# Optimization experiments

Hardware: AMD Instinct MI355X
Metric: run time of the kernel (lower is better)

Reference implementation:

```python
import jax, jax.numpy as jnp
import numpy as np

HEADS = 16
DIM_HEAD = 64
SCALE = DIM_HEAD ** -0.5


def setup_inputs() -> dict:
    key = jax.random.key(0)
    ks = jax.random.split(key, 5)
    dim = 1024
    inner = HEADS * DIM_HEAD  # 1024
    x = jax.random.normal(ks[0], (2, 2048, dim), dtype=jnp.float32)
    # Linear weights stored as [in, out] so y = x @ W
    s = dim ** -0.5
    Wq = jax.random.normal(ks[1], (dim, inner), dtype=jnp.float32) * s
    Wk = jax.random.normal(ks[2], (dim, inner), dtype=jnp.float32) * s
    Wv = jax.random.normal(ks[3], (dim, inner), dtype=jnp.float32) * s
    Wo = jax.random.normal(ks[4], (inner, dim), dtype=jnp.float32) * s
    bo = jnp.zeros((dim,), dtype=jnp.float32)
    return {"x": x, "Wq": Wq, "Wk": Wk, "Wv": Wv, "Wo": Wo, "bo": bo}


def reference(x, Wq, Wk, Wv, Wo, bo):
    b, n, _ = x.shape
    def split_heads(t):  # [b, n, h*d] -> [b, h, n, d]
        return t.reshape(b, n, HEADS, DIM_HEAD).transpose(0, 2, 1, 3)
    q = split_heads(x @ Wq)
    k = split_heads(x @ Wk)
    v = split_heads(x @ Wv)
    sim = jnp.einsum('bhid,bhjd->bhij', q, k) * SCALE  # [b, h, n, n]
    attn = jax.nn.softmax(sim, axis=-1)
    out = jnp.einsum('bhij,bhjd->bhid', attn, v)  # [b, h, n, d]
    out = out.transpose(0, 2, 1, 3).reshape(b, n, HEADS * DIM_HEAD)
    return out @ Wo + bo
```

## Files before the change

### kernel.cpp

```cpp
#include <hip/hip_runtime.h>
#include <hip/hip_fp16.h>

typedef _Float16 f16;
typedef __attribute__((ext_vector_type(8))) _Float16 half8;
typedef __attribute__((ext_vector_type(2))) __fp16 fp16x2_native;
typedef __attribute__((ext_vector_type(4))) float floatx4;
typedef __attribute__((ext_vector_type(16))) float f32x16;
typedef __attribute__((ext_vector_type(4))) unsigned uint4v;
typedef __attribute__((ext_vector_type(2))) unsigned uint2v;

static constexpr int DIM = 1024;
static constexpr int SEQ = 2048;
static constexpr int DH = 64;
static constexpr int MTOT = 4096;

__device__ __forceinline__ float fexp2(float x) {
#if __has_builtin(__builtin_amdgcn_exp2f)
  return __builtin_amdgcn_exp2f(x);
#else
  return exp2f(x);
#endif
}

__device__ __forceinline__ unsigned pkrtz(float a, float b) {
  fp16x2_native h = __builtin_amdgcn_cvt_pkrtz(a, b);
  return __builtin_bit_cast(unsigned, h);
}

__device__ __forceinline__ void pl32swap(unsigned& a, unsigned& b) {
#if __has_builtin(__builtin_amdgcn_permlane32_swap)
  uint2v r = __builtin_amdgcn_permlane32_swap(a, b, false, false);
  a = r.x;
  b = r.y;
#else
  asm volatile("v_permlane32_swap_b32 %0, %1" : "+v"(a), "+v"(b));
#endif
}

__device__ __forceinline__ void gll16(const f16* g, f16* l) {
  auto gp = (__attribute__((address_space(1))) unsigned*)(uintptr_t)(const void*)g;
  auto lp = (__attribute__((address_space(3))) unsigned*)(uintptr_t)(void*)l;
  __builtin_amdgcn_global_load_lds(gp, lp, 16, 0, 0);
}

__global__ __launch_bounds__(256) void k_transpose(
    const float* __restrict__ Wq, const float* __restrict__ Wk,
    const float* __restrict__ Wv, const float* __restrict__ Wo,
    f16* __restrict__ wt)
{
  __shared__ float tile[32][33];
  const int z = blockIdx.z;
  const float* W = (z == 0) ? Wq : (z == 1) ? Wk : (z == 2) ? Wv : Wo;
  f16* out = wt + (size_t)z * DIM * DIM;
  const int tx = threadIdx.x, ty = threadIdx.y;
  const int x0 = blockIdx.x * 32, y0 = blockIdx.y * 32;
#pragma unroll
  for (int i = 0; i < 4; ++i)
    tile[ty + i * 8][tx] = W[(size_t)(y0 + ty + i * 8) * DIM + (x0 + tx)];
  __syncthreads();
#pragma unroll
  for (int i = 0; i < 4; ++i)
    out[(size_t)(x0 + ty + i * 8) * DIM + (y0 + tx)] = (f16)tile[tx][ty + i * 8];
}

__global__ __launch_bounds__(256) void k_xcast(
    const float* __restrict__ in, f16* __restrict__ out)
{
  const int i = blockIdx.x * 256 + threadIdx.x;
  const float4* p = (const float4*)in;
  float4 a = p[2 * i], b = p[2 * i + 1];
  half8 h = {(f16)a.x, (f16)a.y, (f16)a.z, (f16)a.w,
             (f16)b.x, (f16)b.y, (f16)b.z, (f16)b.w};
  *(half8*)(out + (size_t)i * 8) = h;
}

__global__ __launch_bounds__(256) void k_vtrans(
    const f16* __restrict__ vh, f16* __restrict__ vt)
{
  __shared__ f16 T[64][72];
  const int tid = threadIdx.x;
  const int nt = blockIdx.x, bh = blockIdx.y;
  const int b = bh >> 4, h = bh & 15;
  const int n0 = nt * 64;
  const f16* src = vh + (size_t)b * SEQ * DIM + (size_t)h * DH;
#pragma unroll
  for (int i = 0; i < 2; ++i) {
    const int n = (tid >> 3) + i * 32;
    const int cc = tid & 7;
    half8 v = *(const half8*)(src + (size_t)(n0 + n) * DIM + cc * 8);
#pragma unroll
    for (int j = 0; j < 8; ++j) T[cc * 8 + j][n] = v[j];
  }
  __syncthreads();
  f16* dst = vt + (size_t)bh * DH * SEQ;
#pragma unroll
  for (int i = 0; i < 2; ++i) {
    const int d = (tid >> 3) + i * 32;
    const int cc = tid & 7;
    half8 w = *(const half8*)&T[d][cc * 8];
    *(half8*)(dst + (size_t)d * SEQ + n0 + cc * 8) = w;
  }
}

template <bool OUT_F32>
__global__ __launch_bounds__(256) void k_gemm2(
    const f16* __restrict__ A, const f16* __restrict__ BT,
    void* __restrict__ Cptr, const float* __restrict__ bias,
    int M, int N, int K, size_t bt_zstride, size_t c_zstride)
{
  __shared__ f16 SB[2][8192];

  const int tid = threadIdx.x;
  const int lane = tid & 63;
  const int wid = tid >> 6;
  const int wr = (wid >> 1) * 64, wc = (wid & 1) * 64;
  const int li = lane & 15, lg = lane >> 4;

  const f16* BTz = BT + (size_t)blockIdx.z * bt_zstride;
  const int row0 = blockIdx.x * 128, col0 = blockIdx.y * 128;

  const int c0 = tid;
  const int c1 = 256 + tid;
  const f16* a0 = A + (size_t)(row0 + (c0 >> 2)) * K + (c0 & 3) * 8;
  const f16* a1 = A + (size_t)(row0 + (c1 >> 2)) * K + (c1 & 3) * 8;
  const f16* b0 = BTz + (size_t)(col0 + (c0 >> 2)) * K + (c0 & 3) * 8;
  const f16* b1 = BTz + (size_t)(col0 + (c1 >> 2)) * K + (c1 & 3) * 8;
  const int da0 = wid * 512, da1 = 2048 + wid * 512;

  const floatx4 zero4 = {0.f, 0.f, 0.f, 0.f};
  floatx4 acc[4][4];
#pragma unroll
  for (int m = 0; m < 4; ++m)
#pragma unroll
    for (int n = 0; n < 4; ++n) acc[m][n] = zero4;

  auto issue = [&](int buf) {
    gll16(a0, &SB[buf][da0]);
    gll16(a1, &SB[buf][da1]);
    gll16(b0, &SB[buf][4096 + da0]);
    gll16(b1, &SB[buf][4096 + da1]);
    a0 += 32; a1 += 32; b0 += 32; b1 += 32;
  };

  const int nstep = K >> 5;
  issue(0);

  auto step = [&](int buf, int t) {
    asm volatile("s_waitcnt vmcnt(0)" ::: "memory");
    __builtin_amdgcn_s_barrier();
    asm volatile("" ::: "memory");
    if (t + 1 < nstep) issue(buf ^ 1);
    const f16* As = &SB[buf][0];
    const f16* Bs = &SB[buf][4096];
    half8 af[4], bf[4];
#pragma unroll
    for (int m = 0; m < 4; ++m)
      af[m] = *(const half8*)&As[(wr + m * 16 + li) * 32 + lg * 8];
#pragma unroll
    for (int n = 0; n < 4; ++n)
      bf[n] = *(const half8*)&Bs[(wc + n * 16 + li) * 32 + lg * 8];
#pragma unroll
    for (int m = 0; m < 4; ++m)
#pragma unroll
      for (int n = 0; n < 4; ++n)
        acc[m][n] = __builtin_amdgcn_mfma_f32_16x16x32_f16(af[m], bf[n], acc[m][n], 0, 0, 0);
  };

  for (int t2 = 0; t2 < nstep; t2 += 2) {
    step(0, t2);
    step(1, t2 + 1);
  }

#pragma unroll
  for (int m = 0; m < 4; ++m)
#pragma unroll
    for (int n = 0; n < 4; ++n)
#pragma unroll
      for (int r = 0; r < 4; ++r) {
        const int row = row0 + wr + m * 16 + lg * 4 + r;
        const int col = col0 + wc + n * 16 + li;
        if constexpr (OUT_F32) {
          float* C = (float*)Cptr + (size_t)blockIdx.z * c_zstride;
          C[(size_t)row * N + col] = acc[m][n][r] + bias[col];
        } else {
          f16* C = (f16*)Cptr + (size_t)blockIdx.z * c_zstride;
          C[(size_t)row * N + col] = (f16)acc[m][n][r];
        }
      }
}

__global__ __launch_bounds__(256) void k_attn3(
    const f16* __restrict__ qh, const f16* __restrict__ kh,
    const f16* __restrict__ vt, f16* __restrict__ oh)
{
  __shared__ f16 KV[2][8192];
  __shared__ float bc[4][32];

  const int tid = threadIdx.x;
  const int lane = tid & 63;
  const int wid = tid >> 6;
  const int col = lane & 31;
  const int hi = lane >> 5;

  const int id = blockIdx.x;
  const int xcd = id & 7;
  const int j = id >> 3;
  const int bh = xcd * 4 + (j >> 4);
  const int qi = j & 15;
  const int b = bh >> 4, h = bh & 15;

  const int q0 = qi * 128 + wid * 32;
  const size_t xbase = (size_t)b * SEQ * DIM + (size_t)h * DH;
  const size_t vtbase = (size_t)bh * DH * SEQ;

  const float SC = 0.125f * 1.44269504089f;
  const float RTRAW = 8.0f / SC;

  const int c0 = tid;
  const int c1 = 256 + tid;
  const int r0 = c0 >> 3, s0 = ((c0 & 7) ^ (r0 & 7)) * 8;
  const int r1 = c1 >> 3, s1 = ((c1 & 7) ^ (r1 & 7)) * 8;
  const f16* ks0 = kh + xbase + (size_t)r0 * DIM + s0;
  const f16* ks1 = kh + xbase + (size_t)r1 * DIM + s1;
  const f16* vs0 = vt + vtbase + (size_t)r0 * SEQ + s0;
  const f16* vs1 = vt + vtbase + (size_t)r1 * SEQ + s1;
  const int dk0 = wid * 512, dk1 = 2048 + wid * 512;

  auto issue = [&](int buf) {
    gll16(ks0, &KV[buf][dk0]);
    gll16(ks1, &KV[buf][dk1]);
    gll16(vs0, &KV[buf][4096 + dk0]);
    gll16(vs1, &KV[buf][4096 + dk1]);
    ks0 += 64 * DIM; ks1 += 64 * DIM; vs0 += 64; vs1 += 64;
  };

  half8 qb[4];
  {
    const f16* qrow = qh + xbase + (size_t)(q0 + col) * DIM;
#pragma unroll
    for (int s = 0; s < 4; ++s) qb[s] = *(const half8*)(qrow + s * 16 + hi * 8);
  }

  f32x16 o0 = {0, 0, 0, 0, 0, 0, 0, 0, 0, 0, 0, 0, 0, 0, 0, 0};
  f32x16 o1 = {0, 0, 0, 0, 0, 0, 0, 0, 0, 0, 0, 0, 0, 0, 0, 0};
  float m = -1e30f, lsum = 0.f;

  issue(0);

  auto tile = [&](int buf, int t) {
    asm volatile("s_waitcnt vmcnt(0)" ::: "memory");
    __builtin_amdgcn_s_barrier();
    asm volatile("" ::: "memory");
    if (t < 31) issue(buf ^ 1);
    const f16* Ks = &KV[buf][0];
    const f16* Vs = &KV[buf][4096];

#pragma unroll
    for (int kvs = 0; kvs < 2; ++kvs) {
      const int krow = kvs * 32 + col;
      f32x16 sacc = {0, 0, 0, 0, 0, 0, 0, 0, 0, 0, 0, 0, 0, 0, 0, 0};
      __builtin_amdgcn_s_setprio(1);
#pragma unroll
      for (int s = 0; s < 4; ++s) {
        const int cc = (2 * s + hi) ^ (krow & 7);
        half8 ka = *(const half8*)&Ks[krow * 64 + cc * 8];
        sacc = __builtin_amdgcn_mfma_f32_32x32x16_f16(ka, qb[s], sacc, 0, 0, 0);
      }
      __builtin_amdgcn_s_setprio(0);

      float smax = sacc[0];
#pragma unroll
      for (int r = 1; r < 16; ++r) smax = fmaxf(smax, sacc[r]);
      smax = fmaxf(smax, __shfl_xor(smax, 32));

      if (!__all(smax <= m + RTRAW)) {
        const float mn = fmaxf(m, smax);
        const float alpha = fexp2((m - mn) * SC);
        m = mn;
        lsum *= alpha;
        if (hi == 0) bc[wid][col] = alpha;
#pragma unroll
        for (int r = 0; r < 16; ++r) {
          const float a2 = bc[wid][(r & 3) + 8 * (r >> 2) + 4 * hi];
          o0[r] *= a2;
          o1[r] *= a2;
        }
      }

      const float mc = m * SC;
      float pw[16];
      float rs = 0.f;
#pragma unroll
      for (int r = 0; r < 16; ++r) {
        pw[r] = fexp2(fmaf(sacc[r], SC, -mc));
        rs += pw[r];
      }
      rs += __shfl_xor(rs, 32);
      lsum += rs;

      __builtin_amdgcn_s_setprio(1);
#pragma unroll
      for (int s2 = 0; s2 < 2; ++s2) {
        const int rb = s2 * 8;
        unsigned X0 = pkrtz(pw[rb + 0], pw[rb + 1]);
        unsigned X1 = pkrtz(pw[rb + 2], pw[rb + 3]);
        unsigned Y0 = pkrtz(pw[rb + 4], pw[rb + 5]);
        unsigned Y1 = pkrtz(pw[rb + 6], pw[rb + 7]);
        pl32swap(X0, Y0);
        pl32swap(X1, Y1);
        const half8 paf = __builtin_bit_cast(half8, (uint4v){X0, X1, Y0, Y1});
        const int kc = kvs * 4 + s2 * 2 + hi;
#pragma unroll
        for (int dt = 0; dt < 2; ++dt) {
          const int vrow = dt * 32 + col;
          const int cc = kc ^ (vrow & 7);
          half8 vb = *(const half8*)&Vs[vrow * 64 + cc * 8];
          if (dt == 0)
            o0 = __builtin_amdgcn_mfma_f32_32x32x16_f16(paf, vb, o0, 0, 0, 0);
          else
            o1 = __builtin_amdgcn_mfma_f32_32x32x16_f16(paf, vb, o1, 0, 0, 0);
        }
      }
      __builtin_amdgcn_s_setprio(0);
    }
  };

  for (int t2 = 0; t2 < 32; t2 += 2) {
    tile(0, t2);
    tile(1, t2 + 1);
  }

  const float inv = 1.0f / lsum;
  if (hi == 0) bc[wid][col] = inv;
#pragma unroll
  for (int r = 0; r < 16; ++r) {
    const int qr = (r & 3) + 8 * (r >> 2) + 4 * hi;
    const float iv = bc[wid][qr];
    f16* orow = oh + xbase + (size_t)(q0 + qr) * DIM;
    orow[col] = (f16)(o0[r] * iv);
    orow[32 + col] = (f16)(o1[r] * iv);
  }
}

extern "C" void kernel_launch(void* const* d_in, const int* in_sizes, int n_in,
                              void* d_out, int out_size, void* d_ws, size_t ws_size,
                              hipStream_t stream)
{
  const float* x  = (const float*)d_in[0];
  const float* Wq = (const float*)d_in[1];
  const float* Wk = (const float*)d_in[2];
  const float* Wv = (const float*)d_in[3];
  const float* Wo = (const float*)d_in[4];
  const float* bo = (const float*)d_in[5];

  char* ws = (char*)d_ws;
  f16* wt   = (f16*)ws;
  f16* qkvh = (f16*)(ws + (size_t)8 * 1024 * 1024);
  f16* ohp  = (f16*)(ws + (size_t)32 * 1024 * 1024);
  f16* vtb  = (f16*)(ws + (size_t)40 * 1024 * 1024);
  f16* xh   = ohp;

  k_transpose<<<dim3(32, 32, 4), dim3(32, 8), 0, stream>>>(Wq, Wk, Wv, Wo, wt);

  k_xcast<<<2048, 256, 0, stream>>>(x, xh);

  k_gemm2<false><<<dim3(32, 8, 3), 256, 0, stream>>>(
      xh, wt, qkvh, nullptr, MTOT, DIM, DIM,
      (size_t)DIM * DIM, (size_t)MTOT * DIM);

  k_vtrans<<<dim3(32, 32), 256, 0, stream>>>(
      qkvh + (size_t)2 * MTOT * DIM, vtb);

  k_attn3<<<512, 256, 0, stream>>>(
      qkvh, qkvh + (size_t)MTOT * DIM, vtb, ohp);

  k_gemm2<true><<<dim3(32, 8, 1), 256, 0, stream>>>(
      ohp, wt + (size_t)3 * DIM * DIM, d_out, bo, MTOT, DIM, DIM, 0, 0);
}
```

Baseline: 124.0 us.

## Split attention KV range across two wave groups and merge partial softmax

The attention kernel doubles its block to 512 threads. Two groups of four waves each process half of the key/value sequence for the same 128 query rows, with double-buffered shared memory enlarged to hold both halves. Afterwards the partial outputs, maxima and sums are combined through shared memory (split-K style). This is meant to raise wave occupancy and latency hiding on the 512-block grid. The cost is more shared memory, a final merge pass with an extra fp16 rounding of one partial, and a reduction tree rewrite for max and sum.

```diff
diff --git a/kernel.cpp b/kernel.cpp
--- a/kernel.cpp
+++ b/kernel.cpp
@@ -189,16 +189,19 @@
       }
 }
 
-__global__ __launch_bounds__(256) void k_attn3(
+__global__ __launch_bounds__(512) void k_attn4(
     const f16* __restrict__ qh, const f16* __restrict__ kh,
     const f16* __restrict__ vt, f16* __restrict__ oh)
 {
-  __shared__ f16 KV[2][8192];
-  __shared__ float bc[4][32];
+  __shared__ f16 KV[2][16384];
+  __shared__ float bc[8][32];
+  __shared__ float Lm[4][32], Ll[4][32], W0[4][32], W1[4][32];
 
   const int tid = threadIdx.x;
   const int lane = tid & 63;
   const int wid = tid >> 6;
+  const int g = wid >> 2;
+  const int sub = wid & 3;
   const int col = lane & 31;
   const int hi = lane >> 5;
 
@@ -209,28 +212,27 @@
   const int qi = j & 15;
   const int b = bh >> 4, h = bh & 15;
 
-  const int q0 = qi * 128 + wid * 32;
+  const int q0 = qi * 128 + sub * 32;
   const size_t xbase = (size_t)b * SEQ * DIM + (size_t)h * DH;
   const size_t vtbase = (size_t)bh * DH * SEQ;
 
   const float SC = 0.125f * 1.44269504089f;
   const float RTRAW = 8.0f / SC;
 
-  const int c0 = tid;
-  const int c1 = 256 + tid;
-  const int r0 = c0 >> 3, s0 = ((c0 & 7) ^ (r0 & 7)) * 8;
-  const int r1 = c1 >> 3, s1 = ((c1 & 7) ^ (r1 & 7)) * 8;
-  const f16* ks0 = kh + xbase + (size_t)r0 * DIM + s0;
-  const f16* ks1 = kh + xbase + (size_t)r1 * DIM + s1;
-  const f16* vs0 = vt + vtbase + (size_t)r0 * SEQ + s0;
-  const f16* vs1 = vt + vtbase + (size_t)r1 * SEQ + s1;
-  const int dk0 = wid * 512, dk1 = 2048 + wid * 512;
+  const int lc = tid & 511;
+  const int srow = lc >> 3;
+  const int sw = ((lc & 7) ^ (srow & 7)) * 8;
+  const f16* ks0 = kh + xbase + (size_t)srow * DIM + sw;
+  const f16* ks1 = kh + xbase + (size_t)(1024 + srow) * DIM + sw;
+  const f16* vs0 = vt + vtbase + (size_t)srow * SEQ + sw;
+  const f16* vs1 = vt + vtbase + (size_t)srow * SEQ + 1024 + sw;
 
   auto issue = [&](int buf) {
-    gll16(ks0, &KV[buf][dk0]);
-    gll16(ks1, &KV[buf][dk1]);
-    gll16(vs0, &KV[buf][4096 + dk0]);
-    gll16(vs1, &KV[buf][4096 + dk1]);
+    f16* B = &KV[buf][wid * 512];
+    gll16(ks0, B);
+    gll16(vs0, B + 4096);
+    gll16(ks1, B + 8192);
+    gll16(vs1, B + 12288);
     ks0 += 64 * DIM; ks1 += 64 * DIM; vs0 += 64; vs1 += 64;
   };
 
@@ -251,9 +253,9 @@
     asm volatile("s_waitcnt vmcnt(0)" ::: "memory");
     __builtin_amdgcn_s_barrier();
     asm volatile("" ::: "memory");
-    if (t < 31) issue(buf ^ 1);
-    const f16* Ks = &KV[buf][0];
-    const f16* Vs = &KV[buf][4096];
+    if (t < 15) issue(buf ^ 1);
+    const f16* Ks = &KV[buf][g * 8192];
+    const f16* Vs = Ks + 4096;
 
 #pragma unroll
     for (int kvs = 0; kvs < 2; ++kvs) {
@@ -268,9 +270,11 @@
       }
       __builtin_amdgcn_s_setprio(0);
 
-      float smax = sacc[0];
-#pragma unroll
-      for (int r = 1; r < 16; ++r) smax = fmaxf(smax, sacc[r]);
+      float x0 = fmaxf(fmaxf(sacc[0], sacc[1]), fmaxf(sacc[2], sacc[3]));
+      float x1 = fmaxf(fmaxf(sacc[4], sacc[5]), fmaxf(sacc[6], sacc[7]));
+      float x2 = fmaxf(fmaxf(sacc[8], sacc[9]), fmaxf(sacc[10], sacc[11]));
+      float x3 = fmaxf(fmaxf(sacc[12], sacc[13]), fmaxf(sacc[14], sacc[15]));
+      float smax = fmaxf(fmaxf(x0, x1), fmaxf(x2, x3));
       smax = fmaxf(smax, __shfl_xor(smax, 32));
 
       if (!__all(smax <= m + RTRAW)) {
@@ -289,19 +293,20 @@
 
       const float mc = m * SC;
       float pw[16];
-      float rs = 0.f;
-#pragma unroll
-      for (int r = 0; r < 16; ++r) {
-        pw[r] = fexp2(fmaf(sacc[r], SC, -mc));
-        rs += pw[r];
-      }
+#pragma unroll
+      for (int r = 0; r < 16; ++r) pw[r] = fexp2(fmaf(sacc[r], SC, -mc));
+      float s0 = (pw[0] + pw[1]) + (pw[2] + pw[3]);
+      float s1 = (pw[4] + pw[5]) + (pw[6] + pw[7]);
+      float s2 = (pw[8] + pw[9]) + (pw[10] + pw[11]);
+      float s3 = (pw[12] + pw[13]) + (pw[14] + pw[15]);
+      float rs = (s0 + s1) + (s2 + s3);
       rs += __shfl_xor(rs, 32);
       lsum += rs;
 
       __builtin_amdgcn_s_setprio(1);
 #pragma unroll
-      for (int s2 = 0; s2 < 2; ++s2) {
-        const int rb = s2 * 8;
+      for (int s2i = 0; s2i < 2; ++s2i) {
+        const int rb = s2i * 8;
         unsigned X0 = pkrtz(pw[rb + 0], pw[rb + 1]);
         unsigned X1 = pkrtz(pw[rb + 2], pw[rb + 3]);
         unsigned Y0 = pkrtz(pw[rb + 4], pw[rb + 5]);
@@ -309,7 +314,7 @@
         pl32swap(X0, Y0);
         pl32swap(X1, Y1);
         const half8 paf = __builtin_bit_cast(half8, (uint4v){X0, X1, Y0, Y1});
-        const int kc = kvs * 4 + s2 * 2 + hi;
+        const int kc = kvs * 4 + s2i * 2 + hi;
 #pragma unroll
         for (int dt = 0; dt < 2; ++dt) {
           const int vrow = dt * 32 + col;
@@ -325,20 +330,44 @@
     }
   };
 
-  for (int t2 = 0; t2 < 32; t2 += 2) {
+  for (int t2 = 0; t2 < 16; t2 += 2) {
     tile(0, t2);
     tile(1, t2 + 1);
   }
 
   const float inv = 1.0f / lsum;
   if (hi == 0) bc[wid][col] = inv;
-#pragma unroll
-  for (int r = 0; r < 16; ++r) {
-    const int qr = (r & 3) + 8 * (r >> 2) + 4 * hi;
-    const float iv = bc[wid][qr];
-    f16* orow = oh + xbase + (size_t)(q0 + qr) * DIM;
-    orow[col] = (f16)(o0[r] * iv);
-    orow[32 + col] = (f16)(o1[r] * iv);
+  if (g == 1) {
+    if (hi == 0) { Lm[sub][col] = m; Ll[sub][col] = lsum; }
+    f16* po = &KV[0][0] + sub * 2048;
+#pragma unroll
+    for (int r = 0; r < 16; ++r) {
+      const int qr = (r & 3) + 8 * (r >> 2) + 4 * hi;
+      const float iv = bc[wid][qr];
+      po[qr * 64 + col] = (f16)(o0[r] * iv);
+      po[qr * 64 + 32 + col] = (f16)(o1[r] * iv);
+    }
+  }
+  __syncthreads();
+  if (g == 0) {
+    const float m1 = Lm[sub][col], l1 = Ll[sub][col];
+    const float M = fmaxf(m, m1);
+    const float e0 = fexp2((m - M) * SC);
+    const float a0 = lsum * e0;
+    const float a1 = l1 * fexp2((m1 - M) * SC);
+    const float rden = 1.0f / (a0 + a1);
+    const float c0 = e0 * rden;
+    const float w1 = a1 * rden;
+    if (hi == 0) { W0[sub][col] = c0; W1[sub][col] = w1; }
+    const f16* po = &KV[0][0] + sub * 2048;
+#pragma unroll
+    for (int r = 0; r < 16; ++r) {
+      const int qr = (r & 3) + 8 * (r >> 2) + 4 * hi;
+      const float c0r = W0[sub][qr], w1r = W1[sub][qr];
+      f16* orow = oh + xbase + (size_t)(q0 + qr) * DIM;
+      orow[col] = (f16)(c0r * o0[r] + w1r * (float)po[qr * 64 + col]);
+      orow[32 + col] = (f16)(c0r * o1[r] + w1r * (float)po[qr * 64 + 32 + col]);
+    }
   }
 }
 
@@ -371,7 +400,7 @@
   k_vtrans<<<dim3(32, 32), 256, 0, stream>>>(
       qkvh + (size_t)2 * MTOT * DIM, vtb);
 
-  k_attn3<<<512, 256, 0, stream>>>(
+  k_attn4<<<512, 512, 0, stream>>>(
       qkvh, qkvh + (size_t)MTOT * DIM, vtb, ohp);
 
   k_gemm2<true><<<dim3(32, 8, 1), 256, 0, stream>>>(
```

After: 120.7 us. 1.03x faster.

## Split attention over four KV chunks with a merge kernel and head-major output

Applied to the files above, without the earlier changes.

The attention kernel now splits each query tile's KV range into four 512-key chunks, which raises the grid from 512 to 2048 blocks. Each block writes a normalized partial output plus a per-row max and sum, and a new merge kernel combines them into a head-major buffer. The output GEMM gains a head-major A-addressing mode so it can read that layout directly. The aim is better CU occupancy and parallelism for attention, at the cost of an extra kernel launch and extra memory traffic for the partials. Smaller edits swap the LDS alpha and inverse broadcasts for shuffles and turn the max and sum reductions into trees.

```diff
diff --git a/kernel.cpp b/kernel.cpp
--- a/kernel.cpp
+++ b/kernel.cpp
@@ -13,6 +13,7 @@
 static constexpr int SEQ = 2048;
 static constexpr int DH = 64;
 static constexpr int MTOT = 4096;
+static constexpr int QTOT = 65536;
 
 __device__ __forceinline__ float fexp2(float x) {
 #if __has_builtin(__builtin_amdgcn_exp2f)
@@ -102,7 +103,7 @@
   }
 }
 
-template <bool OUT_F32>
+template <bool OUT_F32, bool A_HM>
 __global__ __launch_bounds__(256) void k_gemm2(
     const f16* __restrict__ A, const f16* __restrict__ BT,
     void* __restrict__ Cptr, const float* __restrict__ bias,
@@ -121,8 +122,16 @@
 
   const int c0 = tid;
   const int c1 = 256 + tid;
-  const f16* a0 = A + (size_t)(row0 + (c0 >> 2)) * K + (c0 & 3) * 8;
-  const f16* a1 = A + (size_t)(row0 + (c1 >> 2)) * K + (c1 & 3) * 8;
+  const f16* a0;
+  const f16* a1;
+  if constexpr (A_HM) {
+    const int m0 = row0 + (c0 >> 2), m1 = row0 + (c1 >> 2);
+    a0 = A + (size_t)(m0 >> 11) * 16 * 131072 + (size_t)(m0 & 2047) * 64 + (c0 & 3) * 8;
+    a1 = A + (size_t)(m1 >> 11) * 16 * 131072 + (size_t)(m1 & 2047) * 64 + (c1 & 3) * 8;
+  } else {
+    a0 = A + (size_t)(row0 + (c0 >> 2)) * K + (c0 & 3) * 8;
+    a1 = A + (size_t)(row0 + (c1 >> 2)) * K + (c1 & 3) * 8;
+  }
   const f16* b0 = BTz + (size_t)(col0 + (c0 >> 2)) * K + (c0 & 3) * 8;
   const f16* b1 = BTz + (size_t)(col0 + (c1 >> 2)) * K + (c1 & 3) * 8;
   const int da0 = wid * 512, da1 = 2048 + wid * 512;
@@ -134,12 +143,20 @@
 #pragma unroll
     for (int n = 0; n < 4; ++n) acc[m][n] = zero4;
 
+  int kst = 0;
   auto issue = [&](int buf) {
     gll16(a0, &SB[buf][da0]);
     gll16(a1, &SB[buf][da1]);
     gll16(b0, &SB[buf][4096 + da0]);
     gll16(b1, &SB[buf][4096 + da1]);
-    a0 += 32; a1 += 32; b0 += 32; b1 += 32;
+    if constexpr (A_HM) {
+      const int adv = (kst & 1) ? (131072 - 32) : 32;
+      a0 += adv; a1 += adv;
+      ++kst;
+    } else {
+      a0 += 32; a1 += 32;
+    }
+    b0 += 32; b1 += 32;
   };
 
   const int nstep = K >> 5;
@@ -189,12 +206,12 @@
       }
 }
 
-__global__ __launch_bounds__(256) void k_attn3(
+__global__ __launch_bounds__(256) void k_attn6(
     const f16* __restrict__ qh, const f16* __restrict__ kh,
-    const f16* __restrict__ vt, f16* __restrict__ oh)
+    const f16* __restrict__ vt, f16* __restrict__ p01, f16* __restrict__ p23,
+    float* __restrict__ mArr, float* __restrict__ lArr)
 {
   __shared__ f16 KV[2][8192];
-  __shared__ float bc[4][32];
 
   const int tid = threadIdx.x;
   const int lane = tid & 63;
@@ -205,32 +222,35 @@
   const int id = blockIdx.x;
   const int xcd = id & 7;
   const int j = id >> 3;
-  const int bh = xcd * 4 + (j >> 4);
-  const int qi = j & 15;
+  const int bh = xcd * 4 + (j >> 6);
+  const int rem = j & 63;
+  const int s4 = rem >> 4;
+  const int qi = rem & 15;
   const int b = bh >> 4, h = bh & 15;
 
   const int q0 = qi * 128 + wid * 32;
+  const int kv0 = s4 * 512;
   const size_t xbase = (size_t)b * SEQ * DIM + (size_t)h * DH;
   const size_t vtbase = (size_t)bh * DH * SEQ;
 
   const float SC = 0.125f * 1.44269504089f;
   const float RTRAW = 8.0f / SC;
 
-  const int c0 = tid;
-  const int c1 = 256 + tid;
-  const int r0 = c0 >> 3, s0 = ((c0 & 7) ^ (r0 & 7)) * 8;
-  const int r1 = c1 >> 3, s1 = ((c1 & 7) ^ (r1 & 7)) * 8;
-  const f16* ks0 = kh + xbase + (size_t)r0 * DIM + s0;
-  const f16* ks1 = kh + xbase + (size_t)r1 * DIM + s1;
-  const f16* vs0 = vt + vtbase + (size_t)r0 * SEQ + s0;
-  const f16* vs1 = vt + vtbase + (size_t)r1 * SEQ + s1;
-  const int dk0 = wid * 512, dk1 = 2048 + wid * 512;
+  const int c0 = tid, c1 = tid + 256;
+  const int r0 = c0 >> 3, sw0 = ((c0 & 7) ^ (r0 & 7)) * 8;
+  const int r1 = c1 >> 3, sw1 = ((c1 & 7) ^ (r1 & 7)) * 8;
+  const f16* ks0 = kh + xbase + (size_t)(kv0 + r0) * DIM + sw0;
+  const f16* ks1 = kh + xbase + (size_t)(kv0 + r1) * DIM + sw1;
+  const f16* vs0 = vt + vtbase + (size_t)r0 * SEQ + kv0 + sw0;
+  const f16* vs1 = vt + vtbase + (size_t)r1 * SEQ + kv0 + sw1;
+  const int db0 = wid * 512, db1 = 2048 + wid * 512;
 
   auto issue = [&](int buf) {
-    gll16(ks0, &KV[buf][dk0]);
-    gll16(ks1, &KV[buf][dk1]);
-    gll16(vs0, &KV[buf][4096 + dk0]);
-    gll16(vs1, &KV[buf][4096 + dk1]);
+    f16* B = &KV[buf][0];
+    gll16(ks0, B + db0);
+    gll16(ks1, B + db1);
+    gll16(vs0, B + 4096 + db0);
+    gll16(vs1, B + 4096 + db1);
     ks0 += 64 * DIM; ks1 += 64 * DIM; vs0 += 64; vs1 += 64;
   };
 
@@ -251,7 +271,7 @@
     asm volatile("s_waitcnt vmcnt(0)" ::: "memory");
     __builtin_amdgcn_s_barrier();
     asm volatile("" ::: "memory");
-    if (t < 31) issue(buf ^ 1);
+    if (t < 7) issue(buf ^ 1);
     const f16* Ks = &KV[buf][0];
     const f16* Vs = &KV[buf][4096];
 
@@ -268,9 +288,11 @@
       }
       __builtin_amdgcn_s_setprio(0);
 
-      float smax = sacc[0];
-#pragma unroll
-      for (int r = 1; r < 16; ++r) smax = fmaxf(smax, sacc[r]);
+      float x0 = fmaxf(fmaxf(sacc[0], sacc[1]), fmaxf(sacc[2], sacc[3]));
+      float x1 = fmaxf(fmaxf(sacc[4], sacc[5]), fmaxf(sacc[6], sacc[7]));
+      float x2 = fmaxf(fmaxf(sacc[8], sacc[9]), fmaxf(sacc[10], sacc[11]));
+      float x3 = fmaxf(fmaxf(sacc[12], sacc[13]), fmaxf(sacc[14], sacc[15]));
+      float smax = fmaxf(fmaxf(x0, x1), fmaxf(x2, x3));
       smax = fmaxf(smax, __shfl_xor(smax, 32));
 
       if (!__all(smax <= m + RTRAW)) {
@@ -278,10 +300,9 @@
         const float alpha = fexp2((m - mn) * SC);
         m = mn;
         lsum *= alpha;
-        if (hi == 0) bc[wid][col] = alpha;
 #pragma unroll
         for (int r = 0; r < 16; ++r) {
-          const float a2 = bc[wid][(r & 3) + 8 * (r >> 2) + 4 * hi];
+          const float a2 = __shfl(alpha, (r & 3) + 8 * (r >> 2) + 4 * hi);
           o0[r] *= a2;
           o1[r] *= a2;
         }
@@ -289,19 +310,20 @@
 
       const float mc = m * SC;
       float pw[16];
-      float rs = 0.f;
-#pragma unroll
-      for (int r = 0; r < 16; ++r) {
-        pw[r] = fexp2(fmaf(sacc[r], SC, -mc));
-        rs += pw[r];
-      }
+#pragma unroll
+      for (int r = 0; r < 16; ++r) pw[r] = fexp2(fmaf(sacc[r], SC, -mc));
+      float t0 = (pw[0] + pw[1]) + (pw[2] + pw[3]);
+      float t1 = (pw[4] + pw[5]) + (pw[6] + pw[7]);
+      float t2 = (pw[8] + pw[9]) + (pw[10] + pw[11]);
+      float t3 = (pw[12] + pw[13]) + (pw[14] + pw[15]);
+      float rs = (t0 + t1) + (t2 + t3);
       rs += __shfl_xor(rs, 32);
       lsum += rs;
 
       __builtin_amdgcn_s_setprio(1);
 #pragma unroll
-      for (int s2 = 0; s2 < 2; ++s2) {
-        const int rb = s2 * 8;
+      for (int s2i = 0; s2i < 2; ++s2i) {
+        const int rb = s2i * 8;
         unsigned X0 = pkrtz(pw[rb + 0], pw[rb + 1]);
         unsigned X1 = pkrtz(pw[rb + 2], pw[rb + 3]);
         unsigned Y0 = pkrtz(pw[rb + 4], pw[rb + 5]);
@@ -309,7 +331,7 @@
         pl32swap(X0, Y0);
         pl32swap(X1, Y1);
         const half8 paf = __builtin_bit_cast(half8, (uint4v){X0, X1, Y0, Y1});
-        const int kc = kvs * 4 + s2 * 2 + hi;
+        const int kc = kvs * 4 + s2i * 2 + hi;
 #pragma unroll
         for (int dt = 0; dt < 2; ++dt) {
           const int vrow = dt * 32 + col;
@@ -325,21 +347,66 @@
     }
   };
 
-  for (int t2 = 0; t2 < 32; t2 += 2) {
+  for (int t2 = 0; t2 < 8; t2 += 2) {
     tile(0, t2);
     tile(1, t2 + 1);
   }
 
+  const int gq = bh * 2048 + q0;
   const float inv = 1.0f / lsum;
-  if (hi == 0) bc[wid][col] = inv;
+  if (hi == 0) {
+    mArr[s4 * QTOT + gq + col] = m * SC;
+    lArr[s4 * QTOT + gq + col] = lsum;
+  }
+  f16* pb = (s4 & 2) ? p23 : p01;
+  pb += (size_t)(s4 & 1) * QTOT * DH;
+  f16* prow = pb + (size_t)gq * DH;
 #pragma unroll
   for (int r = 0; r < 16; ++r) {
     const int qr = (r & 3) + 8 * (r >> 2) + 4 * hi;
-    const float iv = bc[wid][qr];
-    f16* orow = oh + xbase + (size_t)(q0 + qr) * DIM;
-    orow[col] = (f16)(o0[r] * iv);
-    orow[32 + col] = (f16)(o1[r] * iv);
-  }
+    const float iv = __shfl(inv, qr);
+    prow[qr * DH + col] = (f16)(o0[r] * iv);
+    prow[qr * DH + 32 + col] = (f16)(o1[r] * iv);
+  }
+}
+
+__global__ __launch_bounds__(256) void k_merge(
+    const f16* __restrict__ p01, const f16* __restrict__ p23,
+    const float* __restrict__ mArr, const float* __restrict__ lArr,
+    f16* __restrict__ out)
+{
+  const int t = blockIdx.x * 256 + threadIdx.x;
+  const int q = t >> 3;
+  const int d8 = (t & 7) * 8;
+
+  float mv[4], lv[4];
+#pragma unroll
+  for (int s = 0; s < 4; ++s) {
+    mv[s] = mArr[s * QTOT + q];
+    lv[s] = lArr[s * QTOT + q];
+  }
+  const float M = fmaxf(fmaxf(mv[0], mv[1]), fmaxf(mv[2], mv[3]));
+  float w[4], den = 0.f;
+#pragma unroll
+  for (int s = 0; s < 4; ++s) {
+    w[s] = lv[s] * fexp2(mv[s] - M);
+    den += w[s];
+  }
+  const float rd = 1.0f / den;
+
+  float a[8] = {0, 0, 0, 0, 0, 0, 0, 0};
+#pragma unroll
+  for (int s = 0; s < 4; ++s) {
+    const f16* pb = (s & 2) ? p23 : p01;
+    pb += (size_t)(s & 1) * QTOT * DH;
+    half8 v = *(const half8*)(pb + (size_t)q * DH + d8);
+#pragma unroll
+    for (int jj = 0; jj < 8; ++jj) a[jj] = fmaf(w[s], (float)v[jj], a[jj]);
+  }
+  half8 o;
+#pragma unroll
+  for (int jj = 0; jj < 8; ++jj) o[jj] = (f16)(a[jj] * rd);
+  *(half8*)(out + (size_t)q * DH + d8) = o;
 }
 
 extern "C" void kernel_launch(void* const* d_in, const int* in_sizes, int n_in,
@@ -360,20 +427,27 @@
   f16* vtb  = (f16*)(ws + (size_t)40 * 1024 * 1024);
   f16* xh   = ohp;
 
+  f16* p01 = (f16*)d_out;
+  f16* p23 = qkvh + (size_t)2 * MTOT * DIM;
+  float* mArr = (float*)ws;
+  float* lArr = (float*)(ws + (size_t)1024 * 1024);
+
   k_transpose<<<dim3(32, 32, 4), dim3(32, 8), 0, stream>>>(Wq, Wk, Wv, Wo, wt);
 
   k_xcast<<<2048, 256, 0, stream>>>(x, xh);
 
-  k_gemm2<false><<<dim3(32, 8, 3), 256, 0, stream>>>(
+  k_gemm2<false, false><<<dim3(32, 8, 3), 256, 0, stream>>>(
       xh, wt, qkvh, nullptr, MTOT, DIM, DIM,
       (size_t)DIM * DIM, (size_t)MTOT * DIM);
 
   k_vtrans<<<dim3(32, 32), 256, 0, stream>>>(
       qkvh + (size_t)2 * MTOT * DIM, vtb);
 
-  k_attn3<<<512, 256, 0, stream>>>(
-      qkvh, qkvh + (size_t)MTOT * DIM, vtb, ohp);
-
-  k_gemm2<true><<<dim3(32, 8, 1), 256, 0, stream>>>(
+  k_attn6<<<2048, 256, 0, stream>>>(
+      qkvh, qkvh + (size_t)MTOT * DIM, vtb, p01, p23, mArr, lArr);
+
+  k_merge<<<2048, 256, 0, stream>>>(p01, p23, mArr, lArr, ohp);
+
+  k_gemm2<true, true><<<dim3(32, 8, 1), 256, 0, stream>>>(
       ohp, wt + (size_t)3 * DIM * DIM, d_out, bo, MTOT, DIM, DIM, 0, 0);
 }
```

Result: slower. 135.4 us (+9.2%).
